# Performance work log

Hardware: AMD Instinct MI355X
Metric: run time of the kernel (lower is better)

## Reference

```python
import jax, jax.numpy as jnp
from jax import lax
import numpy as np


def make_hippo_matrix(N):
    P = np.sqrt(1 + 2 * np.arange(N))
    A = P[:, None] * P[None, :]
    A = np.tril(A) - np.diag(np.arange(N))
    return jnp.asarray(-A, dtype=jnp.float32)


def setup_inputs() -> dict:
    key = jax.random.key(0)
    k1, k2, k3, k4, k5 = jax.random.split(key, 5)
    Bsz, L, H, N = 16, 2048, 512, 64
    dt_min, dt_max = 0.001, 0.1
    u = jax.random.normal(k1, (Bsz, L, H), dtype=jnp.float32)
    B_ssm = jax.random.normal(k2, (N, 1), dtype=jnp.float32)
    C_ssm = jax.random.normal(k3, (1, N), dtype=jnp.float32)
    D_skip = jax.random.normal(k4, (1,), dtype=jnp.float32)
    log_dt = (jax.random.uniform(k5, (1,), dtype=jnp.float32)
              * (np.log(dt_max) - np.log(dt_min)) + np.log(dt_min))
    return {"u": u, "B_ssm": B_ssm, "C_ssm": C_ssm, "D_skip": D_skip, "log_dt": log_dt}


def reference(u, B_ssm, C_ssm, D_skip, log_dt):
    Bsz, L, H = u.shape
    N = B_ssm.shape[0]
    A = make_hippo_matrix(N)  # fixed HiPPO buffer (non-trainable)

    # --- discretize: A_bar = expm(dt*A); B_bar = A^{-1} (A_bar - I) B ---
    dt = jnp.exp(log_dt)  # (1,)
    A_bar = jax.scipy.linalg.expm(dt * A)  # (N, N)
    B_bar = jnp.linalg.solve(A, (A_bar - jnp.eye(N, dtype=A.dtype)) @ B_ssm)  # (N, 1)

    # --- kernel K[k] = C @ A_bar^k @ B_bar, k = 0..L-1, via scan ---
    def step(power, _):
        kk = (C_ssm @ power)[0, 0]
        return A_bar @ power, kk
    _, K = lax.scan(step, B_bar, None, length=L)  # (L,)

    # torch F.conv1d is cross-correlation; with padding L-1 and keeping the
    # first L outputs this equals a causal convolution with the FLIPPED kernel:
    #   y[t] = sum_{m=0}^{t} K[L-1-m] * u[t-m]
    Krev = K[::-1]
    n_fft = 2 * L  # linear (non-circular) convolution
    Uf = jnp.fft.rfft(u, n=n_fft, axis=1)            # (B, n_fft//2+1, H)
    Kf = jnp.fft.rfft(Krev, n=n_fft)                 # (n_fft//2+1,)
    y_conv = jnp.fft.irfft(Uf * Kf[None, :, None], n=n_fft, axis=1)[:, :L, :]
    y = y_conv.astype(u.dtype) + D_skip * u
    return y
```

## Files before the change

kernel.cpp:

```cpp
#include <hip/hip_runtime.h>
#include <math.h>


typedef short short8 __attribute__((ext_vector_type(8)));
typedef float f32x4 __attribute__((ext_vector_type(4)));

#define SWMASK 28
__device__ __forceinline__ int swz(int r, int c) {
  return (r << 6) + (c ^ (r & SWMASK));
}
__device__ __forceinline__ float Aval(int i, int j) {
  if (i > j)  return -(float)(sqrt(2.0 * i + 1.0) * sqrt(2.0 * j + 1.0));
  if (i == j) return -(float)(i + 1);
  return 0.0f;
}
__device__ __forceinline__ unsigned rne_bf16(float x) {
  unsigned u = __float_as_uint(x);
  return (u + 0x7FFFu + ((u >> 16) & 1u)) >> 16;
}
__device__ __forceinline__ float invfact(int k) {
  switch (k) {
    case 0: return 1.0f;            case 1: return 1.0f;
    case 2: return 0.5f;            case 3: return (float)(1.0/6.0);
    case 4: return (float)(1.0/24.0);       case 5: return (float)(1.0/120.0);
    case 6: return (float)(1.0/720.0);      case 7: return (float)(1.0/5040.0);
    case 8: return (float)(1.0/40320.0);    default: return (float)(1.0/362880.0);
  }
}

__device__ __forceinline__ void mm64(float* out, const float* L, const float* R,
                                     const float* Xg, float cI, float cX,
                                     int addG, int tid) {
  __syncthreads();
  const int r0 = (tid & 15) << 2;
  const int c0 = (tid >> 4) << 2;
  const int rm = r0 & SWMASK;
  const int cswz = c0 ^ rm;
  f32x4 acc[4];
#pragma unroll
  for (int i = 0; i < 4; ++i) acc[i] = (f32x4){0.f, 0.f, 0.f, 0.f};

#pragma unroll 8
  for (int k4 = 0; k4 < 64; k4 += 4) {
    const int ka = k4 ^ rm;
    const int cm = c0 ^ (k4 & SWMASK);
    f32x4 a[4], bv[4];
#pragma unroll
    for (int i = 0; i < 4; ++i)
      a[i] = *(const f32x4*)&L[((r0 + i) << 6) + ka];
#pragma unroll
    for (int d = 0; d < 4; ++d)
      bv[d] = *(const f32x4*)&R[((k4 + d) << 6) + cm];
#pragma unroll
    for (int i = 0; i < 4; ++i) {
#pragma unroll
      for (int d = 0; d < 4; ++d)
        acc[i] = a[i][d] * bv[d] + acc[i];
    }
  }
  if (addG) {
#pragma unroll
    for (int i = 0; i < 4; ++i) {
      f32x4 xv = *(const f32x4*)&Xg[((r0 + i) << 6) + cswz];
      acc[i] = cX * xv + acc[i];
#pragma unroll
      for (int j = 0; j < 4; ++j)
        if (r0 + i == c0 + j) acc[i][j] += cI;
    }
  }
#pragma unroll
  for (int i = 0; i < 4; ++i)
    *(f32x4*)&out[((r0 + i) << 6) + cswz] = acc[i];
  __syncthreads();
}

__global__ __launch_bounds__(256) void prep_quant(
    const float* __restrict__ u, const float* __restrict__ B_ssm,
    const float* __restrict__ C_ssm, const float* __restrict__ D_skip,
    const float* __restrict__ log_dt, uint4* __restrict__ rg_hi,
    uint4* __restrict__ rg_lo, int* __restrict__ wsi,
    uint4* __restrict__ ubf) {
  __shared__ __align__(16) float smem[16384];
  const int tid = threadIdx.x;

  if (blockIdx.x != 0) {
    int q = blockIdx.x - 1;
    int b = q >> 7, rem = q & 127;
    int tc = rem >> 1, hf = rem & 1;
    int t0 = (tc << 5) + (hf << 4);
    float* S = smem;
#pragma unroll
    for (int r = 0; r < 8; ++r) {
      int s = tid + (r << 8);
      int row = s >> 7, c4 = (s & 127) << 2;
      float4 v = *(const float4*)(u + ((((b << 11) + t0 + row) << 9) + c4));
      *(float4*)&S[row * 520 + c4] = v;
    }
    __syncthreads();
#pragma unroll
    for (int r = 0; r < 4; ++r) {
      int gidx = tid + (r << 8);
      int jnG = gidx >> 5;
      int gl = (gidx >> 4) & 1;
      int hm = gidx & 15;
      int gg = (hf << 1) | gl;
      int h = (jnG << 4) + hm;
      int tb = gl << 3;
      unsigned pk[4];
#pragma unroll
      for (int q2 = 0; q2 < 4; ++q2) {
        unsigned lo = rne_bf16(S[(tb + 2 * q2) * 520 + h]);
        unsigned hi = rne_bf16(S[(tb + 2 * q2 + 1) * 520 + h]);
        pk[q2] = lo | (hi << 16);
      }
      ubf[(((b << 6) | tc) << 11) | (jnG << 6) | (gg << 4) | hm] =
          make_uint4(pk[0], pk[1], pk[2], pk[3]);
    }
    return;
  }

  float* b0 = smem;
  float* b1 = smem + 4096;
  float* b2 = smem + 8192;
  float* b3 = smem + 12288;
  const int lane = tid & 63, wv = tid >> 6;
  const float dtf = expf(log_dt[0]);

  if (tid < 64) {
    double p = sqrt(2.0 * tid + 1.0);
    double s = p;
#pragma unroll
    for (int off = 1; off < 64; off <<= 1) {
      double t = __shfl_down(s, off, 64);
      if (tid + off < 64) s += t;
    }
    b2[tid] = (float)((tid + 1.0) + p * (s - p));
  }
  __syncthreads();
  float maxc = 0.f;
  for (int j = 0; j < 64; ++j) maxc = fmaxf(maxc, b2[j]);
  int E;
  frexpf(dtf * maxc, &E);
  int sExp = E > 0 ? E : 0;
  const float scale = ldexpf(dtf, -sExp);
  __syncthreads();

  for (int idx = tid; idx < 4096; idx += 256) {
    int r = idx >> 6, c = idx & 63;
    b0[swz(r, c)] = scale * Aval(r, c);
  }
  mm64(b1, b0, b0, b0, 0.f, 0.f, 0, tid);
  for (int idx = tid; idx < 4096; idx += 256) {
    int r = idx >> 6, c = idx & 63;
    float gv = invfact(9) * b0[swz(r, c)];
    if (r == c) gv += invfact(8);
    b2[swz(r, c)] = gv;
  }
  float* Pc = b2;
  float* Pn = b3;
#pragma unroll
  for (int mq = 3; mq >= 0; --mq) {
    mm64(Pn, Pc, b1, b0, invfact(2 * mq), invfact(2 * mq + 1), 1, tid);
    float* t = Pc; Pc = Pn; Pn = t;
  }
  for (int q = 0; q < sExp; ++q) {
    mm64(Pn, Pc, Pc, b0, 0.f, 0.f, 0, tid);
    float* t = Pc; Pc = Pn; Pn = t;
  }
  float* Vt = b0;
  float* Wt = b1 + 256;
  float* Bl = b1 + 2500;
  if (tid < 64) Bl[tid] = B_ssm[tid];
  __syncthreads();

  if (tid < 64) {
    int i = tid;
    double accd = 0.0;
#pragma unroll
    for (int k4 = 0; k4 < 16; ++k4) {
      int jM = (k4 << 2) ^ (i & 28);
      float4 mv = *(const float4*)&Pc[(i << 6) + jM];
      float4 bv = *(const float4*)&Bl[k4 << 2];
      accd += (double)mv.x * bv.x + (double)mv.y * bv.y +
              (double)mv.z * bv.z + (double)mv.w * bv.w;
    }
    accd -= (double)Bl[i];
    double xv = 0.0;
    for (int j = 0; j < 64; ++j) {
      if (i == j) xv = accd / (double)Aval(j, j);
      double xj = __shfl(xv, j, 64);
      if (i > j) accd -= (double)Aval(i, j) * xj;
    }
    Vt[i] = (float)xv;
  }
  __syncthreads();

  for (int k = 0; k < 6; ++k) {
    int cnt = 1 << k;
    for (int t = wv; t < cnt; t += 4) {
      float accv = 0.f;
#pragma unroll
      for (int k4 = 0; k4 < 16; ++k4) {
        int jM = (k4 << 2) ^ (lane & 28);
        float4 mv = *(const float4*)&Pc[(lane << 6) + jM];
        float4 vvv = *(const float4*)&Vt[t * 68 + (k4 << 2)];
        accv += mv.x * vvv.x + mv.y * vvv.y + mv.z * vvv.z + mv.w * vvv.w;
      }
      Vt[(t + cnt) * 68 + lane] = accv;
    }
    mm64(Pn, Pc, Pc, b0, 0.f, 0.f, 0, tid);
    float* t2 = Pc; Pc = Pn; Pn = t2;
  }
  for (int idx = tid; idx < 4096; idx += 256) {
    int r = idx >> 6, c = idx & 63;
    Pn[swz(c, r)] = Pc[swz(r, c)];
  }
  __syncthreads();
  { float* t2 = Pc; Pc = Pn; Pn = t2; }
  if (tid < 64) Wt[lane] = C_ssm[lane];
  __syncthreads();
  for (int k = 0; k < 5; ++k) {
    int cnt = 1 << k;
    for (int t = wv; t < cnt; t += 4) {
      float accv = 0.f;
#pragma unroll
      for (int k4 = 0; k4 < 16; ++k4) {
        int jM = (k4 << 2) ^ (lane & 28);
        float4 mv = *(const float4*)&Pc[(lane << 6) + jM];
        float4 wvv = *(const float4*)&Wt[t * 68 + (k4 << 2)];
        accv += mv.x * wvv.x + mv.y * wvv.y + mv.z * wvv.z + mv.w * wvv.w;
      }
      Wt[(t + cnt) * 68 + lane] = accv;
    }
    if (k < 4) {
      mm64(Pn, Pc, Pc, b0, 0.f, 0.f, 0, tid);
      float* t2 = Pc; Pc = Pn; Pn = t2;
    } else {
      __syncthreads();
    }
  }

  float* K = Pn;
  for (int x = tid; x < 2048; x += 256) {
    int tp = x >> 6, t = x & 63;
    float dot = 0.f;
#pragma unroll
    for (int i4 = 0; i4 < 64; i4 += 4) {
      float4 wvv = *(const float4*)&Wt[tp * 68 + i4];
      float4 vvv = *(const float4*)&Vt[t * 68 + i4];
      dot += wvv.x * vvv.x + wvv.y * vvv.y + wvv.z * vvv.z + wvv.w * vvv.w;
    }
    K[x] = dot;
  }
  __syncthreads();

  unsigned short* kh = (unsigned short*)Pc;
  unsigned short* kl = kh + 2192;
  float* ss = (float*)(kh + 4400);
  const float D = D_skip[0];
  for (int x = tid; x < 2192; x += 256) {
    float v = 0.f;
    if (x < 2048) { v = K[x]; if (x == 2047) v += D; }
    unsigned h = rne_bf16(v);
    float hf2 = __uint_as_float(h << 16);
    unsigned l = rne_bf16(v - hf2);
    kh[x] = (unsigned short)h;
    kl[x] = (unsigned short)l;
  }
  {
    float ssum = 0.f;
#pragma unroll
    for (int q = 0; q < 8; ++q) {
      int x = (tid << 3) + q;
      float v = K[x];
      if (x == 2047) v += D;
      ssum += v * v;
    }
    ss[tid] = ssum;
  }
  __syncthreads();

  for (int e = tid; e < 2176; e += 256) {
    unsigned ph[4], pl[4];
#pragma unroll
    for (int q2 = 0; q2 < 4; ++q2) {
      ph[q2] = (unsigned)kh[e + 2 * q2] | ((unsigned)kh[e + 2 * q2 + 1] << 16);
      pl[q2] = (unsigned)kl[e + 2 * q2] | ((unsigned)kl[e + 2 * q2 + 1] << 16);
    }
    rg_hi[e] = make_uint4(ph[0], ph[1], ph[2], ph[3]);
    rg_lo[e] = make_uint4(pl[0], pl[1], pl[2], pl[3]);
  }
  if (tid == 0) {
    float accq = 0.f;
    int xt = 0;
    for (int jc = 255; jc >= 0; --jc) {
      float na = accq + ss[jc];
      if (na > 4e-8f) { xt = (jc + 1) << 3; break; }
      accq = na;
    }
    wsi[0] = 2048 - xt;
  }
}

__device__ __forceinline__ void load_bfrag(short8* bf, const uint4* ubf,
                                           const float* u, int use_ubf, int b,
                                           int kt, int h0, int wn, int lane) {
  if (use_ubf) {
    const short8* base = (const short8*)(ubf + ((((b << 6) | kt) << 11) |
                                               (((h0 >> 4) + (wn << 2)) << 6) |
                                               lane));
#pragma unroll
    for (int j = 0; j < 4; ++j) bf[j] = base[j << 6];
  } else {
    int gg = lane >> 4, hm = lane & 15;
#pragma unroll
    for (int j = 0; j < 4; ++j) {
      const float* src = u + ((((b << 11) + (kt << 5) + (gg << 3)) << 9) + h0 +
                              (((wn << 2) + j) << 4) + hm);
      unsigned pk[4];
#pragma unroll
      for (int q = 0; q < 4; ++q) {
        unsigned lo = rne_bf16(src[q << 10]);
        unsigned hi = rne_bf16(src[(q << 10) + 512]);
        pk[q] = lo | (hi << 16);
      }
      uint4 vv = make_uint4(pk[0], pk[1], pk[2], pk[3]);
      bf[j] = __builtin_bit_cast(short8, vv);
    }
  }
}

__global__ __launch_bounds__(256) void conv_kernel(
    const float* __restrict__ u, const uint4* __restrict__ rg_hi,
    const uint4* __restrict__ rg_lo, const uint4* __restrict__ ubf,
    const int* __restrict__ wsi, float* __restrict__ y, int use_ubf) {
  __shared__ __align__(16) unsigned ringh[1024], ringl[1024];
  const int tid = threadIdx.x;
  const int bid = blockIdx.x;
  const int b = bid >> 5;
  const int bn = bid & 3;
  const int pr = (bid >> 2) & 7;
  const int h0 = bn << 7;
  const int lane = tid & 63, w = tid >> 6;
  const int wm = w & 1, wn = w >> 1;
  const int g = lane >> 4, m = lane & 15;
  const int D_lo = wsi[0];

  for (int tile = 0; tile < 2; ++tile) {
    const int bm = tile ? pr : 15 - pr;
    const int l0 = bm << 7;
    const int e0 = 1920 - l0;
    const int ktiles = 4 * bm + 4;
    int kt_lim = ((l0 + 127 - D_lo) >> 5) + 1;
    if (kt_lim < 0) kt_lim = 0;
    if (kt_lim > ktiles) kt_lim = ktiles;

    __syncthreads();
    for (int tsk = tid; tsk < 432; tsk += 256) {
      int isLo = tsk >= 216;
      int e = e0 + (isLo ? tsk - 216 : tsk);
      if (e <= 2175) {
        uint4 v = isLo ? rg_lo[e] : rg_hi[e];
        ((uint4*)(isLo ? ringl : ringh))[e & 255] = v;
      }
    }

    f32x4 acc[4][4];
#pragma unroll
    for (int i = 0; i < 4; ++i)
#pragma unroll
      for (int j = 0; j < 4; ++j) acc[i][j] = (f32x4){0.f, 0.f, 0.f, 0.f};

    short8 bcur[4];
    if (kt_lim > 0) load_bfrag(bcur, ubf, u, use_ubf, b, 0, h0, wn, lane);

    for (int kt = 0; kt < kt_lim; ++kt) {
      __syncthreads();
      uint4 tv;
      bool tdo = false;
      int tslot = 0;
      const bool tlo = (tid >= 32);
      if (tid < 64) {
        int te = e0 + 216 + (kt << 5) + (tid & 31);
        if (te <= 2175) {
          tv = tlo ? rg_lo[te] : rg_hi[te];
          tdo = true;
          tslot = te & 255;
        }
      }
      const int ebase = 2047 - l0 + (kt << 5) - (wm << 6) - m + (g << 3);
      short8 ah[4], al[4];
#pragma unroll
      for (int i = 0; i < 4; ++i) {
        int slot = (ebase - (i << 4)) & 255;
        ah[i] = ((const short8*)ringh)[slot];
        al[i] = ((const short8*)ringl)[slot];
      }
      short8 bnx[4];
      if (kt + 1 < kt_lim)
        load_bfrag(bnx, ubf, u, use_ubf, b, kt + 1, h0, wn, lane);
#pragma unroll
      for (int i = 0; i < 4; ++i)
#pragma unroll
        for (int j = 0; j < 4; ++j) {
          acc[i][j] = __builtin_amdgcn_mfma_f32_16x16x32_bf16(ah[i], bcur[j],
                                                              acc[i][j], 0, 0, 0);
          acc[i][j] = __builtin_amdgcn_mfma_f32_16x16x32_bf16(al[i], bcur[j],
                                                              acc[i][j], 0, 0, 0);
        }
      if (tdo) ((uint4*)(tlo ? ringl : ringh))[tslot] = tv;
      if (kt + 1 < kt_lim) {
#pragma unroll
        for (int j = 0; j < 4; ++j) bcur[j] = bnx[j];
      }
    }

#pragma unroll
    for (int i = 0; i < 4; ++i)
#pragma unroll
      for (int j = 0; j < 4; ++j) {
        int l = l0 + (wm << 6) + (i << 4) + (g << 2);
        int h = h0 + (((wn << 2) + j) << 4) + m;
        int off = (((b << 11) + l) << 9) + h;
#pragma unroll
        for (int r = 0; r < 4; ++r) y[off + (r << 9)] = acc[i][j][r];
      }
  }
}

extern "C" void kernel_launch(void* const* d_in, const int* in_sizes, int n_in,
                              void* d_out, int out_size, void* d_ws,
                              size_t ws_size, hipStream_t stream) {
  (void)in_sizes; (void)n_in; (void)out_size;
  const float* u = (const float*)d_in[0];
  const float* B_ssm = (const float*)d_in[1];
  const float* C_ssm = (const float*)d_in[2];
  const float* D_skip = (const float*)d_in[3];
  const float* log_dt = (const float*)d_in[4];
  float* y = (float*)d_out;

  const size_t UBF_BYTES = (size_t)16 * 64 * 2048 * 16;
  const size_t RG_BYTES = (size_t)2176 * 16 * 2 + 256;
  int use_ubf = (ws_size >= UBF_BYTES + RG_BYTES) ? 1 : 0;
  char* wsb = (char*)d_ws;
  uint4* ubf = (uint4*)wsb;
  uint4* rg_hi = use_ubf ? (uint4*)(wsb + UBF_BYTES) : (uint4*)wsb;
  uint4* rg_lo = rg_hi + 2176;
  int* wsi = (int*)(rg_lo + 2176);

  prep_quant<<<use_ubf ? 2049 : 1, 256, 0, stream>>>(
      u, B_ssm, C_ssm, D_skip, log_dt, rg_hi, rg_lo, wsi, ubf);
  conv_kernel<<<512, 256, 0, stream>>>(u, rg_hi, rg_lo, ubf, wsi, y, use_ubf);
}
```

Baseline: 232.7 us.

## Compute matrix exponential and power chain with split-bf16 MFMA matmuls

Replaces the scalar fp32 64x64 shared-memory matmul used in the Taylor/squaring expm and the A_bar power chain with MFMA bf16 matmuls using a hi/lo split (three MFMAs per product) to keep near-fp32 accuracy. Matrices are kept in both row- and column-major bf16 pair layouts so each step can emit the transposed result directly, and the squaring now tracks A_bar - I to preserve precision. This targets the serial single-block setup phase in prep_quant; the risk is reduced accuracy in K from the split-bf16 approximation and the restructured expm.

After: 218.4 us. 6.2% less time.

```diff
diff --git a/kernel.cpp b/kernel.cpp
--- a/kernel.cpp
+++ b/kernel.cpp
@@ -3,6 +3,7 @@
 
 
 typedef short short8 __attribute__((ext_vector_type(8)));
+typedef short short4v __attribute__((ext_vector_type(4)));
 typedef float f32x4 __attribute__((ext_vector_type(4)));
 
 #define SWMASK 28
@@ -27,50 +28,132 @@
     case 8: return (float)(1.0/40320.0);    default: return (float)(1.0/362880.0);
   }
 }
-
-__device__ __forceinline__ void mm64(float* out, const float* L, const float* R,
-                                     const float* Xg, float cI, float cX,
-                                     int addG, int tid) {
-  __syncthreads();
-  const int r0 = (tid & 15) << 2;
-  const int c0 = (tid >> 4) << 2;
-  const int rm = r0 & SWMASK;
-  const int cswz = c0 ^ rm;
-  f32x4 acc[4];
-#pragma unroll
-  for (int i = 0; i < 4; ++i) acc[i] = (f32x4){0.f, 0.f, 0.f, 0.f};
-
-#pragma unroll 8
-  for (int k4 = 0; k4 < 64; k4 += 4) {
-    const int ka = k4 ^ rm;
-    const int cm = c0 ^ (k4 & SWMASK);
-    f32x4 a[4], bv[4];
-#pragma unroll
-    for (int i = 0; i < 4; ++i)
-      a[i] = *(const f32x4*)&L[((r0 + i) << 6) + ka];
-#pragma unroll
-    for (int d = 0; d < 4; ++d)
-      bv[d] = *(const f32x4*)&R[((k4 + d) << 6) + cm];
-#pragma unroll
-    for (int i = 0; i < 4; ++i) {
-#pragma unroll
-      for (int d = 0; d < 4; ++d)
-        acc[i] = a[i][d] * bv[d] + acc[i];
-    }
-  }
-  if (addG) {
-#pragma unroll
-    for (int i = 0; i < 4; ++i) {
-      f32x4 xv = *(const f32x4*)&Xg[((r0 + i) << 6) + cswz];
-      acc[i] = cX * xv + acc[i];
-#pragma unroll
-      for (int j = 0; j < 4; ++j)
-        if (r0 + i == c0 + j) acc[i][j] += cI;
-    }
-  }
-#pragma unroll
-  for (int i = 0; i < 4; ++i)
-    *(f32x4*)&out[((r0 + i) << 6) + cswz] = acc[i];
+__device__ __forceinline__ int slotU(int row, int kg) {
+  return (row << 6) + ((kg ^ (row & 7)) << 3);
+}
+__device__ __forceinline__ float bf2f(unsigned short s) {
+  return __uint_as_float(((unsigned)s) << 16);
+}
+__device__ __forceinline__ unsigned short bfh(float x) {
+  return (unsigned short)rne_bf16(x);
+}
+__device__ __forceinline__ unsigned short bfl(float x, unsigned short h) {
+  return (unsigned short)rne_bf16(x - __uint_as_float(((unsigned)h) << 16));
+}
+
+__device__ __forceinline__ void mmMFMA(
+    const unsigned short* rowLh, const unsigned short* rowLl,
+    const unsigned short* colRh, const unsigned short* colRl,
+    unsigned short* oColH, unsigned short* oColL,
+    unsigned short* oRowH, unsigned short* oRowL,
+    float* oF32, const float* Xg, float cI, float cX, int tid) {
+  const int lane = tid & 63, w = tid >> 6;
+  const int g = lane >> 4, m = lane & 15;
+  const bool doN = (oColH != nullptr) || (oF32 != nullptr);
+  const bool doT = (oRowH != nullptr);
+  f32x4 an[4], at[4];
+
+  if (doN) {
+    short8 ah[2], al[2];
+#pragma unroll
+    for (int kt = 0; kt < 2; ++kt) {
+      ah[kt] = *(const short8*)&rowLh[slotU(16 * w + m, 4 * kt + g)];
+      al[kt] = *(const short8*)&rowLl[slotU(16 * w + m, 4 * kt + g)];
+    }
+#pragma unroll
+    for (int nt = 0; nt < 4; ++nt) {
+      an[nt] = (f32x4){0.f, 0.f, 0.f, 0.f};
+#pragma unroll
+      for (int kt = 0; kt < 2; ++kt) {
+        short8 bh = *(const short8*)&colRh[slotU(16 * nt + m, 4 * kt + g)];
+        short8 bl = *(const short8*)&colRl[slotU(16 * nt + m, 4 * kt + g)];
+        an[nt] = __builtin_amdgcn_mfma_f32_16x16x32_bf16(ah[kt], bh, an[nt], 0, 0, 0);
+        an[nt] = __builtin_amdgcn_mfma_f32_16x16x32_bf16(ah[kt], bl, an[nt], 0, 0, 0);
+        an[nt] = __builtin_amdgcn_mfma_f32_16x16x32_bf16(al[kt], bh, an[nt], 0, 0, 0);
+      }
+      if (Xg) {
+#pragma unroll
+        for (int r = 0; r < 4; ++r) {
+          int rc = 16 * w + 4 * g + r, cc = 16 * nt + m;
+          float gv = cX * Xg[(rc << 6) + (cc ^ (rc & 28))];
+          if (rc == cc) gv += cI;
+          an[nt][r] += gv;
+        }
+      }
+    }
+  }
+  if (doT) {
+    short8 ah[2], al[2];
+#pragma unroll
+    for (int kt = 0; kt < 2; ++kt) {
+      ah[kt] = *(const short8*)&colRh[slotU(16 * w + m, 4 * kt + g)];
+      al[kt] = *(const short8*)&colRl[slotU(16 * w + m, 4 * kt + g)];
+    }
+#pragma unroll
+    for (int nt = 0; nt < 4; ++nt) {
+      at[nt] = (f32x4){0.f, 0.f, 0.f, 0.f};
+#pragma unroll
+      for (int kt = 0; kt < 2; ++kt) {
+        short8 bh = *(const short8*)&rowLh[slotU(16 * nt + m, 4 * kt + g)];
+        short8 bl = *(const short8*)&rowLl[slotU(16 * nt + m, 4 * kt + g)];
+        at[nt] = __builtin_amdgcn_mfma_f32_16x16x32_bf16(ah[kt], bh, at[nt], 0, 0, 0);
+        at[nt] = __builtin_amdgcn_mfma_f32_16x16x32_bf16(ah[kt], bl, at[nt], 0, 0, 0);
+        at[nt] = __builtin_amdgcn_mfma_f32_16x16x32_bf16(al[kt], bh, at[nt], 0, 0, 0);
+      }
+      if (Xg) {
+        int rc = 16 * nt + m;
+        int cb = 16 * w + 4 * g;
+        f32x4 xv = *(const f32x4*)&Xg[(rc << 6) + (cb ^ (rc & 28))];
+#pragma unroll
+        for (int r = 0; r < 4; ++r) {
+          float gv = cX * xv[r];
+          if (rc == cb + r) gv += cI;
+          at[nt][r] += gv;
+        }
+      }
+    }
+  }
+  __syncthreads();
+  const int k0 = 16 * w + 4 * g;
+  if (doN) {
+#pragma unroll
+    for (int nt = 0; nt < 4; ++nt) {
+      if (oColH) {
+        short4v h4, l4;
+#pragma unroll
+        for (int r = 0; r < 4; ++r) {
+          unsigned short h = bfh(an[nt][r]);
+          h4[r] = (short)h;
+          l4[r] = (short)bfl(an[nt][r], h);
+        }
+        int s = slotU(16 * nt + m, k0 >> 3) + (k0 & 7);
+        *(short4v*)&oColH[s] = h4;
+        *(short4v*)&oColL[s] = l4;
+      }
+      if (oF32) {
+#pragma unroll
+        for (int r = 0; r < 4; ++r) {
+          int rc = k0 + r;
+          oF32[(rc << 6) + ((16 * nt + m) ^ (rc & 28))] = an[nt][r];
+        }
+      }
+    }
+  }
+  if (doT) {
+#pragma unroll
+    for (int nt = 0; nt < 4; ++nt) {
+      short4v h4, l4;
+#pragma unroll
+      for (int r = 0; r < 4; ++r) {
+        unsigned short h = bfh(at[nt][r]);
+        h4[r] = (short)h;
+        l4[r] = (short)bfl(at[nt][r], h);
+      }
+      int s = slotU(16 * nt + m, k0 >> 3) + (k0 & 7);
+      *(short4v*)&oRowH[s] = h4;
+      *(short4v*)&oRowL[s] = l4;
+    }
+  }
   __syncthreads();
 }
 
@@ -123,6 +206,12 @@
   float* b1 = smem + 4096;
   float* b2 = smem + 8192;
   float* b3 = smem + 12288;
+  unsigned short* RH = (unsigned short*)b2;
+  unsigned short* RL = RH + 4096;
+  unsigned short* CH = (unsigned short*)b3;
+  unsigned short* CL = CH + 4096;
+  unsigned short* X2H = (unsigned short*)b1;
+  unsigned short* X2L = X2H + 4096;
   const int lane = tid & 63, wv = tid >> 6;
   const float dtf = expf(log_dt[0]);
 
@@ -139,38 +228,82 @@
   __syncthreads();
   float maxc = 0.f;
   for (int j = 0; j < 64; ++j) maxc = fmaxf(maxc, b2[j]);
-  int E;
-  frexpf(dtf * maxc, &E);
-  int sExp = E > 0 ? E : 0;
+  int iE;
+  frexpf(dtf * maxc, &iE);
+  int sExp = iE > 0 ? iE : 0;
   const float scale = ldexpf(dtf, -sExp);
   __syncthreads();
 
-  for (int idx = tid; idx < 4096; idx += 256) {
-    int r = idx >> 6, c = idx & 63;
-    b0[swz(r, c)] = scale * Aval(r, c);
-  }
-  mm64(b1, b0, b0, b0, 0.f, 0.f, 0, tid);
-  for (int idx = tid; idx < 4096; idx += 256) {
-    int r = idx >> 6, c = idx & 63;
-    float gv = invfact(9) * b0[swz(r, c)];
-    if (r == c) gv += invfact(8);
-    b2[swz(r, c)] = gv;
-  }
-  float* Pc = b2;
-  float* Pn = b3;
-#pragma unroll
-  for (int mq = 3; mq >= 0; --mq) {
-    mm64(Pn, Pc, b1, b0, invfact(2 * mq), invfact(2 * mq + 1), 1, tid);
-    float* t = Pc; Pc = Pn; Pn = t;
-  }
-  for (int q = 0; q < sExp; ++q) {
-    mm64(Pn, Pc, Pc, b0, 0.f, 0.f, 0, tid);
-    float* t = Pc; Pc = Pn; Pn = t;
-  }
-  float* Vt = b0;
-  float* Wt = b1 + 256;
-  float* Bl = b1 + 2500;
-  if (tid < 64) Bl[tid] = B_ssm[tid];
+  const int r0i = (tid & 15) << 2, c0i = (tid >> 4) << 2;
+  float xv[4][4];
+  unsigned short xh[4][4], xl[4][4];
+#pragma unroll
+  for (int i = 0; i < 4; ++i)
+#pragma unroll
+    for (int j = 0; j < 4; ++j) {
+      float x = scale * Aval(r0i + i, c0i + j);
+      xv[i][j] = x;
+      xh[i][j] = bfh(x);
+      xl[i][j] = bfl(x, xh[i][j]);
+      b0[swz(r0i + i, c0i + j)] = x;
+    }
+#pragma unroll
+  for (int i = 0; i < 4; ++i) {
+    short4v h4, l4;
+#pragma unroll
+    for (int j = 0; j < 4; ++j) { h4[j] = (short)xh[i][j]; l4[j] = (short)xl[i][j]; }
+    int s = slotU(r0i + i, c0i >> 3) + (c0i & 7);
+    *(short4v*)&RH[s] = h4;
+    *(short4v*)&RL[s] = l4;
+  }
+#pragma unroll
+  for (int j = 0; j < 4; ++j) {
+    short4v h4, l4;
+#pragma unroll
+    for (int i = 0; i < 4; ++i) { h4[i] = (short)xh[i][j]; l4[i] = (short)xl[i][j]; }
+    int s = slotU(c0i + j, r0i >> 3) + (r0i & 7);
+    *(short4v*)&CH[s] = h4;
+    *(short4v*)&CL[s] = l4;
+  }
+  __syncthreads();
+
+  mmMFMA(RH, RL, CH, CL, X2H, X2L, nullptr, nullptr, nullptr, nullptr,
+         0.f, 0.f, tid);
+
+#pragma unroll
+  for (int i = 0; i < 4; ++i) {
+    short4v h4, l4;
+#pragma unroll
+    for (int j = 0; j < 4; ++j) {
+      float gv = invfact(9) * xv[i][j];
+      if (r0i + i == c0i + j) gv += invfact(8);
+      unsigned short h = bfh(gv);
+      h4[j] = (short)h;
+      l4[j] = (short)bfl(gv, h);
+    }
+    int s = slotU(r0i + i, c0i >> 3) + (c0i & 7);
+    *(short4v*)&RH[s] = h4;
+    *(short4v*)&RL[s] = l4;
+  }
+  __syncthreads();
+
+  for (int mq = 3; mq >= 1; --mq)
+    mmMFMA(RH, RL, X2H, X2L, nullptr, nullptr, RH, RL, nullptr, b0,
+           invfact(2 * mq), invfact(2 * mq + 1), tid);
+  mmMFMA(RH, RL, X2H, X2L, CH, CL, RH, RL, b1, b0, 0.f, 1.f, tid);
+
+  for (int q = 0; q < sExp; ++q)
+    mmMFMA(RH, RL, CH, CL, CH, CL, RH, RL, b1, b1, 0.f, 2.f, tid);
+
+  float* Bl = b0 + 64;
+  if (tid < 64) {
+    Bl[tid] = B_ssm[tid];
+    int d = tid;
+    float x = b1[(d << 6) + (d ^ (d & 28))] + 1.0f;
+    unsigned short h = bfh(x), l = bfl(x, h);
+    int s = slotU(d, d >> 3) + (d & 7);
+    RH[s] = h; RL[s] = l; CH[s] = h; CL[s] = l;
+  }
   __syncthreads();
 
   if (tid < 64) {
@@ -179,19 +312,18 @@
 #pragma unroll
     for (int k4 = 0; k4 < 16; ++k4) {
       int jM = (k4 << 2) ^ (i & 28);
-      float4 mv = *(const float4*)&Pc[(i << 6) + jM];
+      float4 mv = *(const float4*)&b1[(i << 6) + jM];
       float4 bv = *(const float4*)&Bl[k4 << 2];
       accd += (double)mv.x * bv.x + (double)mv.y * bv.y +
               (double)mv.z * bv.z + (double)mv.w * bv.w;
     }
-    accd -= (double)Bl[i];
-    double xv = 0.0;
+    double xvv = 0.0;
     for (int j = 0; j < 64; ++j) {
-      if (i == j) xv = accd / (double)Aval(j, j);
-      double xj = __shfl(xv, j, 64);
+      if (i == j) xvv = accd / (double)Aval(j, j);
+      double xj = __shfl(xvv, j, 64);
       if (i > j) accd -= (double)Aval(i, j) * xj;
     }
-    Vt[i] = (float)xv;
+    b0[i] = (float)xvv;
   }
   __syncthreads();
 
@@ -200,61 +332,71 @@
     for (int t = wv; t < cnt; t += 4) {
       float accv = 0.f;
 #pragma unroll
-      for (int k4 = 0; k4 < 16; ++k4) {
-        int jM = (k4 << 2) ^ (lane & 28);
-        float4 mv = *(const float4*)&Pc[(lane << 6) + jM];
-        float4 vvv = *(const float4*)&Vt[t * 68 + (k4 << 2)];
-        accv += mv.x * vvv.x + mv.y * vvv.y + mv.z * vvv.z + mv.w * vvv.w;
-      }
-      Vt[(t + cnt) * 68 + lane] = accv;
-    }
-    mm64(Pn, Pc, Pc, b0, 0.f, 0.f, 0, tid);
-    float* t2 = Pc; Pc = Pn; Pn = t2;
-  }
-  for (int idx = tid; idx < 4096; idx += 256) {
-    int r = idx >> 6, c = idx & 63;
-    Pn[swz(c, r)] = Pc[swz(r, c)];
-  }
-  __syncthreads();
-  { float* t2 = Pc; Pc = Pn; Pn = t2; }
-  if (tid < 64) Wt[lane] = C_ssm[lane];
+      for (int kg = 0; kg < 8; ++kg) {
+        short8 mh = *(const short8*)&RH[slotU(lane, kg)];
+        short8 ml = *(const short8*)&RL[slotU(lane, kg)];
+        f32x4 v0 = *(const f32x4*)&b0[(t << 6) + ((kg << 3) ^ (t & 28))];
+        f32x4 v1 = *(const f32x4*)&b0[(t << 6) + (((kg << 3) + 4) ^ (t & 28))];
+#pragma unroll
+        for (int j = 0; j < 4; ++j)
+          accv += (bf2f((unsigned short)mh[j]) + bf2f((unsigned short)ml[j])) * v0[j];
+#pragma unroll
+        for (int j = 0; j < 4; ++j)
+          accv += (bf2f((unsigned short)mh[4 + j]) + bf2f((unsigned short)ml[4 + j])) * v1[j];
+      }
+      int td = t + cnt;
+      b0[(td << 6) + (lane ^ (td & 28))] = accv;
+    }
+    mmMFMA(RH, RL, CH, CL, CH, CL, RH, RL, nullptr, nullptr, 0.f, 0.f, tid);
+  }
+
+  if (tid < 64) b1[tid] = C_ssm[tid];
   __syncthreads();
   for (int k = 0; k < 5; ++k) {
     int cnt = 1 << k;
     for (int t = wv; t < cnt; t += 4) {
       float accv = 0.f;
 #pragma unroll
-      for (int k4 = 0; k4 < 16; ++k4) {
-        int jM = (k4 << 2) ^ (lane & 28);
-        float4 mv = *(const float4*)&Pc[(lane << 6) + jM];
-        float4 wvv = *(const float4*)&Wt[t * 68 + (k4 << 2)];
-        accv += mv.x * wvv.x + mv.y * wvv.y + mv.z * wvv.z + mv.w * wvv.w;
-      }
-      Wt[(t + cnt) * 68 + lane] = accv;
-    }
-    if (k < 4) {
-      mm64(Pn, Pc, Pc, b0, 0.f, 0.f, 0, tid);
-      float* t2 = Pc; Pc = Pn; Pn = t2;
+      for (int kg = 0; kg < 8; ++kg) {
+        short8 ch8 = *(const short8*)&CH[slotU(lane, kg)];
+        short8 cl8 = *(const short8*)&CL[slotU(lane, kg)];
+        f32x4 w0 = *(const f32x4*)&b1[(t << 6) + (kg << 3)];
+        f32x4 w1 = *(const f32x4*)&b1[(t << 6) + (kg << 3) + 4];
+#pragma unroll
+        for (int j = 0; j < 4; ++j)
+          accv += (bf2f((unsigned short)ch8[j]) + bf2f((unsigned short)cl8[j])) * w0[j];
+#pragma unroll
+        for (int j = 0; j < 4; ++j)
+          accv += (bf2f((unsigned short)ch8[4 + j]) + bf2f((unsigned short)cl8[4 + j])) * w1[j];
+      }
+      b1[((t + cnt) << 6) + lane] = accv;
+    }
+    if (k < 3) {
+      mmMFMA(RH, RL, CH, CL, CH, CL, RH, RL, nullptr, nullptr, 0.f, 0.f, tid);
+    } else if (k == 3) {
+      mmMFMA(RH, RL, CH, CL, CH, CL, nullptr, nullptr, nullptr, nullptr,
+             0.f, 0.f, tid);
     } else {
       __syncthreads();
     }
   }
 
-  float* K = Pn;
+  float* K = b3;
   for (int x = tid; x < 2048; x += 256) {
     int tp = x >> 6, t = x & 63;
     float dot = 0.f;
 #pragma unroll
     for (int i4 = 0; i4 < 64; i4 += 4) {
-      float4 wvv = *(const float4*)&Wt[tp * 68 + i4];
-      float4 vvv = *(const float4*)&Vt[t * 68 + i4];
-      dot += wvv.x * vvv.x + wvv.y * vvv.y + wvv.z * vvv.z + wvv.w * vvv.w;
+      f32x4 wv4 = *(const f32x4*)&b1[(tp << 6) + i4];
+      f32x4 vv4 = *(const f32x4*)&b0[(t << 6) + (i4 ^ (t & 28))];
+      dot += wv4[0] * vv4[0] + wv4[1] * vv4[1] + wv4[2] * vv4[2] +
+             wv4[3] * vv4[3];
     }
     K[x] = dot;
   }
   __syncthreads();
 
-  unsigned short* kh = (unsigned short*)Pc;
+  unsigned short* kh = (unsigned short*)b2;
   unsigned short* kl = kh + 2192;
   float* ss = (float*)(kh + 4400);
   const float D = D_skip[0];
```
